# Kernel tuning notes

Measured on AMD Instinct MI355X. Metric: run time of the kernel, lower is better.

The kernel has to match this reference:

```python
import jax, jax.numpy as jnp
import numpy as np

D_MODEL = 1024
N_HEADS = 16
D_HEAD = D_MODEL // N_HEADS
SCALE = 1.0 / (D_HEAD ** 0.5)


def _rel_shift(t):
    # Transformer-XL relative shift: pad -> view -> slice -> view. t: [b,h,q,k]
    b, h, q, k = t.shape
    padded = jnp.pad(t, ((0, 0), (0, 0), (0, 0), (1, 0)))  # [b,h,q,k+1]
    shifted = padded.reshape(b, h, k + 1, q)[:, :, 1:, :].reshape(b, h, q, k)
    return shifted


def setup_inputs() -> dict:
    key = jax.random.key(0)
    ks = jax.random.split(key, 10)
    B, T, M = 2, 1024, 1024
    J = M + T
    inp = {
        "x": jax.random.normal(ks[0], (B, T, D_MODEL), dtype=jnp.float32),
        "memory": jax.random.normal(ks[1], (B, M, D_MODEL), dtype=jnp.float32),
        "pos_emb": jax.random.normal(ks[2], (J, D_MODEL), dtype=jnp.float32),
        # nn.Linear(d, d, bias=False) weights: y = x @ W.T, W: [out, in]
        "q_w": jax.random.normal(ks[3], (D_MODEL, D_MODEL), dtype=jnp.float32) * 0.02,
        "k_w": jax.random.normal(ks[4], (D_MODEL, D_MODEL), dtype=jnp.float32) * 0.02,
        "v_w": jax.random.normal(ks[5], (D_MODEL, D_MODEL), dtype=jnp.float32) * 0.02,
        "r_w": jax.random.normal(ks[6], (D_MODEL, D_MODEL), dtype=jnp.float32) * 0.02,
        "out_w": jax.random.normal(ks[7], (D_MODEL, D_MODEL), dtype=jnp.float32) * 0.02,
        "pos_bias_u": jax.random.normal(ks[8], (N_HEADS, D_HEAD), dtype=jnp.float32) * 0.02,
        "pos_bias_v": jax.random.normal(ks[9], (N_HEADS, D_HEAD), dtype=jnp.float32) * 0.02,
    }
    return inp


def reference(x, memory, pos_emb, q_w, k_w, v_w, r_w, out_w, pos_bias_u, pos_bias_v):
    B, T, _ = x.shape
    cat = jnp.concatenate([memory, x], axis=1)  # [B, M+T, d]
    L = cat.shape[1]

    def heads(t):  # [B, time, d] -> [B, h, time, dh]
        return t.reshape(t.shape[0], t.shape[1], N_HEADS, D_HEAD).transpose(0, 2, 1, 3)

    q = heads(x @ q_w.T)      # [B,h,T,dh]
    k = heads(cat @ k_w.T)    # [B,h,L,dh]
    v = heads(cat @ v_w.T)    # [B,h,L,dh]
    r = (pos_emb @ r_w.T).reshape(-1, N_HEADS, D_HEAD).transpose(1, 0, 2)  # [h,J,dh]

    q_u = q + pos_bias_u[None, :, None, :]
    q_v = q + pos_bias_v[None, :, None, :]

    content_score = jnp.einsum('bhqd,bhkd->bhqk', q_u, k)  # [B,h,T,L]
    rel_score = jnp.einsum('bhqd,hjd->bhqj', q_v, r)        # [B,h,T,J]
    rel_score = _rel_shift(rel_score)

    scores = (content_score + rel_score) * SCALE
    attn = jax.nn.softmax(scores, axis=-1)
    out = jnp.einsum('bhqk,bhkd->bhqd', attn, v)            # [B,h,T,dh]
    out = out.transpose(0, 2, 1, 3).reshape(B, T, N_HEADS * D_HEAD)
    return out @ out_w.T
```

## Files before the change

kernel.cpp:

```cpp
#include <hip/hip_runtime.h>


typedef unsigned short u16;
typedef unsigned int u32;
typedef short bf16x8 __attribute__((ext_vector_type(8)));
typedef float f32x4 __attribute__((ext_vector_type(4)));

#define MFMA16(a, b, c) __builtin_amdgcn_mfma_f32_16x16x32_bf16(a, b, c, 0, 0, 0)

__device__ __forceinline__ u16 f2bf(float f) {
  u32 u = __float_as_uint(f);
  u32 r = (u + 0x7fffu + ((u >> 16) & 1u)) >> 16;
  return (u16)r;
}

__device__ __forceinline__ void async16(void* lds, const void* g) {
  __builtin_amdgcn_global_load_lds(
      (const __attribute__((address_space(1))) u32*)g,
      (__attribute__((address_space(3))) u32*)lds, 16, 0, 0);
}

__global__ void prep_kernel(const float* __restrict__ x, const float* __restrict__ mem,
                            const float* __restrict__ pos,
                            const float* __restrict__ qw, const float* __restrict__ kw,
                            const float* __restrict__ vw, const float* __restrict__ rw,
                            const float* __restrict__ ow,
                            u16* __restrict__ catb, u16* __restrict__ posb,
                            u16* __restrict__ wqb, u16* __restrict__ wkb,
                            u16* __restrict__ wvb, u16* __restrict__ wrb,
                            u16* __restrict__ wob) {
  const int seg = blockIdx.y;
  const int vid = blockIdx.x * blockDim.x + threadIdx.x;
  const float* src = nullptr;
  u16* dst = nullptr;
  int count = 0;
  switch (seg) {
    case 0: count = (2 * 2048 * 1024) / 4; dst = catb; break;
    case 1: count = (2048 * 1024) / 4; src = pos; dst = posb; break;
    case 2: count = (1024 * 1024) / 4; src = qw; dst = wqb; break;
    case 3: count = (1024 * 1024) / 4; src = kw; dst = wkb; break;
    case 4: count = (1024 * 1024) / 4; src = vw; dst = wvb; break;
    case 5: count = (1024 * 1024) / 4; src = rw; dst = wrb; break;
    case 6: count = (1024 * 1024) / 4; src = ow; dst = wob; break;
  }
  if (vid >= count) return;
  float4 f;
  if (seg == 0) {
    int e = vid * 4;
    int col = e & 1023;
    int row = (e >> 10) & 2047;
    int b = e >> 21;
    const float* s2 = (row < 1024)
                          ? (mem + ((size_t)(b * 1024 + row) * 1024 + col))
                          : (x + ((size_t)(b * 1024 + (row - 1024)) * 1024 + col));
    f = *(const float4*)s2;
  } else {
    f = *(const float4*)(src + (size_t)vid * 4);
  }
  ushort4 o4;
  o4.x = f2bf(f.x); o4.y = f2bf(f.y); o4.z = f2bf(f.z); o4.w = f2bf(f.w);
  *(ushort4*)(dst + (size_t)vid * 4) = o4;
}

__device__ __forceinline__ void gemm_core(const u16* __restrict__ A, const u16* __restrict__ W,
                                          u16* As, u16* Bs, int m0, int n0, bool qmap,
                                          f32x4 acc[4][4]) {
  const int t = threadIdx.x;
  const int lane = t & 63, wid = t >> 6;
  const int colL = lane & 15, rg = lane >> 4;
  const int wm = (wid >> 1) * 64, wn = (wid & 1) * 64;
  for (int kt = 0; kt < 32; ++kt) {
    __syncthreads();
#pragma unroll
    for (int pass = 0; pass < 2; ++pass) {
      int slot = t + pass * 256;
      int row = slot >> 2, ch = slot & 3;
      int sch = ch ^ ((row >> 1) & 3);
      int ar = m0 + row;
      if (qmap) ar = ((ar >> 10) << 11) + 1024 + (ar & 1023);
      async16(As + slot * 8, A + (size_t)ar * 1024 + kt * 32 + sch * 8);
      async16(Bs + slot * 8, W + (size_t)(n0 + row) * 1024 + kt * 32 + sch * 8);
    }
    __syncthreads();
    bf16x8 af[4], bfr[4];
#pragma unroll
    for (int mi = 0; mi < 4; ++mi) {
      int r = wm + mi * 16 + colL;
      af[mi] = *(const bf16x8*)(As + r * 32 + (rg ^ ((r >> 1) & 3)) * 8);
    }
#pragma unroll
    for (int ni = 0; ni < 4; ++ni) {
      int r = wn + ni * 16 + colL;
      bfr[ni] = *(const bf16x8*)(Bs + r * 32 + (rg ^ ((r >> 1) & 3)) * 8);
    }
#pragma unroll
    for (int mi = 0; mi < 4; ++mi)
#pragma unroll
      for (int ni = 0; ni < 4; ++ni)
        acc[mi][ni] = MFMA16(af[mi], bfr[ni], acc[mi][ni]);
  }
}

__global__ __launch_bounds__(256, 2) void gemm_qkvr(
    const u16* __restrict__ catb, const u16* __restrict__ posb,
    const u16* __restrict__ wqb, const u16* __restrict__ wrb,
    const u16* __restrict__ wkb, const u16* __restrict__ wvb,
    const float* __restrict__ bu, const float* __restrict__ bv,
    u16* __restrict__ qub, u16* __restrict__ qvb, u16* __restrict__ rbuf,
    u16* __restrict__ kbuf, u16* __restrict__ vtbuf) {
  __shared__ u16 As[128 * 32], Bs[128 * 32];
  __shared__ u16 Ep[4][16 * 72];
  const int x = blockIdx.x;
  const int bid = (x & 7) * 96 + (x >> 3);
  const u16* A;
  const u16* W;
  int mode, r2;
  bool qmap = false;
  if (bid < 128)      { mode = 0; A = catb; W = wqb; qmap = true; r2 = bid; }
  else if (bid < 256) { mode = 1; A = posb; W = wrb; r2 = bid - 128; }
  else if (bid < 512) { mode = 2; A = catb; W = wkb; r2 = bid - 256; }
  else                { mode = 3; A = catb; W = wvb; r2 = bid - 512; }
  const int m0 = (r2 >> 3) * 128, n0 = (r2 & 7) * 128;
  f32x4 acc[4][4];
  f32x4 zz = {0.f, 0.f, 0.f, 0.f};
#pragma unroll
  for (int a1 = 0; a1 < 4; ++a1)
#pragma unroll
    for (int a2 = 0; a2 < 4; ++a2) acc[a1][a2] = zz;
  gemm_core(A, W, As, Bs, m0, n0, qmap, acc);
  const int t = threadIdx.x, lane = t & 63, wid = t >> 6;
  const int colL = lane & 15, rg = lane >> 4;
  const int wm = (wid >> 1) * 64, wn = (wid & 1) * 64;
  const float sc = 0.18033688f;
  if (mode == 3) {
    u16* Ew = &Ep[wid][0];
    const int bb = m0 >> 11;
    const int j0w = (m0 + wm) & 2047;
    const int hh = (n0 + wn) >> 6;
    const size_t vb0 =
        (((size_t)(bb * 16 + hh) * 32 + (j0w >> 6)) * 4) * 1024;
#pragma unroll
    for (int ni = 0; ni < 4; ++ni) {
#pragma unroll
      for (int mi = 0; mi < 4; ++mi) {
        u32 lo = (u32)f2bf(acc[mi][ni][0]) | ((u32)f2bf(acc[mi][ni][1]) << 16);
        u32 hi = (u32)f2bf(acc[mi][ni][2]) | ((u32)f2bf(acc[mi][ni][3]) << 16);
        uint2 pk; pk.x = lo; pk.y = hi;
        *(uint2*)(Ew + colL * 72 + mi * 16 + rg * 4) = pk;
      }
      asm volatile("s_waitcnt lgkmcnt(0)" ::: "memory");
      const size_t vb = vb0 + (size_t)ni * 1024;
#pragma unroll
      for (int rr = 0; rr < 2; ++rr) {
        int ch = rr * 4 + rg;
        int dr = colL;
        bf16x8 vv = *(const bf16x8*)(Ew + dr * 72 + ch * 8);
        *(bf16x8*)(vtbuf + vb + ch * 128 + dr * 8) = vv;
      }
      asm volatile("s_waitcnt lgkmcnt(0)" ::: "memory");
    }
    return;
  }
#pragma unroll
  for (int mi = 0; mi < 4; ++mi)
#pragma unroll
    for (int ni = 0; ni < 4; ++ni)
#pragma unroll
      for (int e = 0; e < 4; ++e) {
        int m = m0 + wm + mi * 16 + rg * 4 + e;
        int n = n0 + wn + ni * 16 + colL;
        float val = acc[mi][ni][e];
        int hh = n >> 6, dd = n & 63;
        if (mode == 0) {
          int bb = m >> 10, tq = m & 1023;
          size_t ad = (((size_t)(bb * 16 + hh)) * 1024 + tq) * 64 + dd;
          qub[ad] = f2bf((val + bu[n]) * sc);
          qvb[ad] = f2bf((val + bv[n]) * sc);
        } else if (mode == 1) {
          rbuf[((((size_t)hh * 128 + (m >> 4)) * 8 + (dd >> 3)) * 16 + (m & 15)) * 8 +
               (dd & 7)] = f2bf(val);
        } else {
          int bb = m >> 11, j = m & 2047;
          size_t bh2 = (size_t)(bb * 16 + hh);
          kbuf[(((bh2 * 128 + (j >> 4)) * 8 + (dd >> 3)) * 16 + (j & 15)) * 8 + (dd & 7)] =
              f2bf(val);
        }
      }
}

__global__ __launch_bounds__(256, 2) void attn_kernel(
    const u16* __restrict__ qu, const u16* __restrict__ qv, const u16* __restrict__ ktile,
    const u16* __restrict__ vtile, const u16* __restrict__ rtile,
    float* __restrict__ opart, float* __restrict__ mlpart) {
  __shared__ float Ulds[4][3200];
  const int t = threadIdx.x;
  const int wid = t >> 6, lane = t & 63;
  const int colL = lane & 15, rg = lane >> 4;
  const int bid = ((blockIdx.x & 7) << 6) | (blockIdx.x >> 3);
  const int bh = bid >> 4;
  const int rem = bid & 15;
  const int qc = rem >> 1, ks = rem & 1;
  const int h = bh & 15;
  const int i0 = qc * 128 + wid * 32;

  const u16* qub = qu + (size_t)bh * (1024 * 64);
  const u16* qvb = qv + (size_t)bh * (1024 * 64);
  const u16* kb = ktile + (size_t)bh * (128 * 1024);
  const u16* vb = vtile + (size_t)bh * (32 * 4096);
  const u16* rb = rtile + (size_t)h * (128 * 1024);
  const int lane8 = (rg * 16 + colL) * 8;

  bf16x8 aqu0[2], aqv0[2], aqu1[2], aqv1[2];
  {
    int r0 = i0 + colL;
    int r1 = i0 + 16 + colL;
#pragma unroll
    for (int kx = 0; kx < 2; ++kx) {
      aqu0[kx] = *(const bf16x8*)(qub + (size_t)r0 * 64 + kx * 32 + rg * 8);
      aqv0[kx] = *(const bf16x8*)(qvb + (size_t)r0 * 64 + kx * 32 + rg * 8);
      aqu1[kx] = *(const bf16x8*)(qub + (size_t)r1 * 64 + kx * 32 + rg * 8);
      aqv1[kx] = *(const bf16x8*)(qvb + (size_t)r1 * 64 + kx * 32 + rg * 8);
    }
  }
  bf16x8 ones;
#pragma unroll
  for (int i = 0; i < 8; ++i) ones[i] = (short)0x3F80;

  const f32x4 zz = {0.f, 0.f, 0.f, 0.f};
  f32x4 o0[4], o1[4];
  f32x4 lacc0 = zz, lacc1 = zz;
#pragma unroll
  for (int e = 0; e < 4; ++e) { o0[e] = zz; o1[e] = zz; }
  int lb0[4], lb1[4];
#pragma unroll
  for (int e = 0; e < 4; ++e) {
    lb0[e] = (rg * 4 + e) * 99 + colL + 31;
    lb1[e] = (rg * 4 + e) * 99 + colL + 1615;
  }

  float* Uw = &Ulds[wid][0];
  u16* Pw = (u16*)Uw;

#pragma unroll 1
  for (int jt = ks * 16; jt < ks * 16 + 16; ++jt) {
    const int j0 = jt * 64;
    f32x4 s0[4], s1[4];
    __builtin_amdgcn_s_setprio(1);
#pragma unroll
    for (int ni = 0; ni < 4; ++ni) {
      const u16* kp = kb + (size_t)((j0 >> 4) + ni) * 1024 + lane8;
      bf16x8 b0 = *(const bf16x8*)kp;
      bf16x8 b1 = *(const bf16x8*)(kp + 512);
      s0[ni] = zz;
      s0[ni] = MFMA16(aqu0[0], b0, s0[ni]);
      s0[ni] = MFMA16(aqu0[1], b1, s0[ni]);
      s1[ni] = zz;
      s1[ni] = MFMA16(aqu1[0], b0, s1[ni]);
      s1[ni] = MFMA16(aqu1[1], b1, s1[ni]);
    }
    __builtin_amdgcn_s_setprio(0);
    const int pbase2 = j0 + 992 - i0;
    const bool mainv = (pbase2 <= 2047);
    const bool leak = (pbase2 + 94 >= 2049);
    if (mainv) {
      const int tb = pbase2 >> 4;
      bf16x8 rc[12];
#pragma unroll
      for (int uc = 0; uc < 6; ++uc) {
        int tt = tb + uc;
        tt = tt < 127 ? tt : 127;
        const u16* rp = rb + (size_t)tt * 1024 + lane8;
        rc[2 * uc] = *(const bf16x8*)rp;
        rc[2 * uc + 1] = *(const bf16x8*)(rp + 512);
      }
      __builtin_amdgcn_s_setprio(1);
#pragma unroll
      for (int uc = 1; uc < 6; ++uc) {
        f32x4 ua = zz;
        ua = MFMA16(aqv0[0], rc[2 * uc], ua);
        ua = MFMA16(aqv0[1], rc[2 * uc + 1], ua);
#pragma unroll
        for (int e = 0; e < 4; ++e) Uw[(rg * 4 + e) * 100 + uc * 16 + colL] = ua[e];
      }
#pragma unroll
      for (int uc = 0; uc < 5; ++uc) {
        f32x4 ub = zz;
        ub = MFMA16(aqv1[0], rc[2 * uc], ub);
        ub = MFMA16(aqv1[1], rc[2 * uc + 1], ub);
#pragma unroll
        for (int e = 0; e < 4; ++e) Uw[(16 + rg * 4 + e) * 100 + uc * 16 + colL] = ub[e];
      }
      __builtin_amdgcn_s_setprio(0);
      asm volatile("s_waitcnt lgkmcnt(0)" ::: "memory");
      const int pl0 = pbase2 + colL + 31;
      const int pl1 = pbase2 + colL + 15;
#pragma unroll
      for (int c = 0; c < 4; ++c)
#pragma unroll
        for (int e = 0; e < 4; ++e) {
          int w0e = rg * 4 + e;
          float u0 = Uw[lb0[e] + c * 16];
          float u1 = Uw[lb1[e] + c * 16];
          int p0 = pl0 + c * 16 - w0e;
          int p1 = pl1 + c * 16 - w0e;
          s0[c][e] += (p0 <= 2047) ? u0 : 0.f;
          s1[c][e] += (p1 <= 2047) ? u1 : 0.f;
        }
    }
    if (leak) {
      asm volatile("s_waitcnt lgkmcnt(0)" ::: "memory");
      bf16x8 aqs0[2], aqs1[2];
      {
        int rs0 = i0 + colL + 1;
        int rs1 = i0 + 16 + colL + 1;
        rs1 = rs1 < 1024 ? rs1 : 1023;
#pragma unroll
        for (int kx = 0; kx < 2; ++kx) {
          aqs0[kx] = *(const bf16x8*)(qvb + (size_t)rs0 * 64 + kx * 32 + rg * 8);
          aqs1[kx] = *(const bf16x8*)(qvb + (size_t)rs1 * 64 + kx * 32 + rg * 8);
        }
      }
      const int mB1 = (pbase2 - 2048) >> 4;
      const int rowL = (colL + 15) & 15;
      const int tadj = (colL > 0) ? 0 : -1;
      bf16x8 r2[12];
#pragma unroll
      for (int uc = 0; uc < 6; ++uc) {
        int tL = mB1 + uc + tadj;
        tL = tL < 0 ? 0 : (tL > 127 ? 127 : tL);
        const u16* rp = rb + (size_t)tL * 1024 + rg * 128 + rowL * 8;
        r2[2 * uc] = *(const bf16x8*)rp;
        r2[2 * uc + 1] = *(const bf16x8*)(rp + 512);
      }
      __builtin_amdgcn_s_setprio(1);
#pragma unroll
      for (int uc = 1; uc < 6; ++uc) {
        f32x4 ua = zz;
        ua = MFMA16(aqs0[0], r2[2 * uc], ua);
        ua = MFMA16(aqs0[1], r2[2 * uc + 1], ua);
#pragma unroll
        for (int e = 0; e < 4; ++e) Uw[(rg * 4 + e) * 100 + uc * 16 + colL] = ua[e];
      }
#pragma unroll
      for (int uc = 0; uc < 5; ++uc) {
        f32x4 ub = zz;
        ub = MFMA16(aqs1[0], r2[2 * uc], ub);
        ub = MFMA16(aqs1[1], r2[2 * uc + 1], ub);
#pragma unroll
        for (int e = 0; e < 4; ++e) Uw[(16 + rg * 4 + e) * 100 + uc * 16 + colL] = ub[e];
      }
      __builtin_amdgcn_s_setprio(0);
      asm volatile("s_waitcnt lgkmcnt(0)" ::: "memory");
      const int pl0 = pbase2 + colL + 31;
      const int pl1 = pbase2 + colL + 15;
#pragma unroll
      for (int c = 0; c < 4; ++c)
#pragma unroll
        for (int e = 0; e < 4; ++e) {
          int w0e = rg * 4 + e;
          int p0 = pl0 + c * 16 - w0e;
          int p1 = pl1 + c * 16 - w0e;
          if (p0 >= 2049) s0[c][e] += Uw[lb0[e] + c * 16];
          if (p1 >= 2049) s1[c][e] += Uw[lb1[e] + c * 16];
        }
    }
    bf16x8 vf[8];
    {
      const u16* vp0 = vb + (size_t)jt * 4096 + lane8;
#pragma unroll
      for (int ni = 0; ni < 4; ++ni) {
        vf[2 * ni] = *(const bf16x8*)(vp0 + ni * 1024);
        vf[2 * ni + 1] = *(const bf16x8*)(vp0 + ni * 1024 + 512);
      }
    }
#pragma unroll
    for (int c = 0; c < 4; ++c)
#pragma unroll
      for (int e = 0; e < 4; ++e) {
        int row = rg * 4 + e;
        int col = c * 16 + colL;
        int sw = (col >> 3) ^ (row & 7);
        float p0 = __builtin_amdgcn_exp2f(s0[c][e] - 16.0f);
        float p1 = __builtin_amdgcn_exp2f(s1[c][e] - 16.0f);
        Pw[row * 64 + sw * 8 + (colL & 7)] = f2bf(p0);
        Pw[(16 + row) * 64 + sw * 8 + (colL & 7)] = f2bf(p1);
      }
    asm volatile("s_waitcnt lgkmcnt(0)" ::: "memory");
    bf16x8 pa0[2], pa1[2];
#pragma unroll
    for (int kx = 0; kx < 2; ++kx) {
      int chunk = kx * 4 + rg;
      int sw = chunk ^ (colL & 7);
      pa0[kx] = *(const bf16x8*)(Pw + colL * 64 + sw * 8);
      pa1[kx] = *(const bf16x8*)(Pw + (16 + colL) * 64 + sw * 8);
    }
    __builtin_amdgcn_s_setprio(1);
    lacc0 = MFMA16(pa0[0], ones, lacc0);
    lacc0 = MFMA16(pa0[1], ones, lacc0);
    lacc1 = MFMA16(pa1[0], ones, lacc1);
    lacc1 = MFMA16(pa1[1], ones, lacc1);
#pragma unroll
    for (int ni = 0; ni < 4; ++ni) {
      o0[ni] = MFMA16(pa0[0], vf[2 * ni], o0[ni]);
      o0[ni] = MFMA16(pa0[1], vf[2 * ni + 1], o0[ni]);
      o1[ni] = MFMA16(pa1[0], vf[2 * ni], o1[ni]);
      o1[ni] = MFMA16(pa1[1], vf[2 * ni + 1], o1[ni]);
    }
    __builtin_amdgcn_s_setprio(0);
    asm volatile("" ::: "memory");
  }
  const size_t rowbase = (size_t)ks * 32768 + (size_t)bh * 1024 + i0;
#pragma unroll
  for (int c = 0; c < 4; ++c)
#pragma unroll
    for (int e = 0; e < 4; ++e) {
      int row = rg * 4 + e;
      opart[(rowbase + row) * 64 + c * 16 + colL] = o0[c][e];
      opart[(rowbase + 16 + row) * 64 + c * 16 + colL] = o1[c][e];
    }
  if (colL == 0) {
#pragma unroll
    for (int e = 0; e < 4; ++e) {
      size_t r = rowbase + rg * 4 + e;
      mlpart[r * 2 + 0] = 16.0f;
      mlpart[r * 2 + 1] = lacc0[e];
      mlpart[(r + 16) * 2 + 0] = 16.0f;
      mlpart[(r + 16) * 2 + 1] = lacc1[e];
    }
  }
}

__global__ void combine_kernel(const float* __restrict__ opart,
                               const float* __restrict__ mlpart,
                               u16* __restrict__ aout) {
  const int gid = blockIdx.x * 256 + threadIdx.x;
  const int r = gid >> 4;
  const int cg = gid & 15;
  float2 ml0 = *(const float2*)(mlpart + (size_t)r * 2);
  float2 ml1 = *(const float2*)(mlpart + ((size_t)32768 + r) * 2);
  float m = fmaxf(ml0.x, ml1.x);
  float f0 = __builtin_amdgcn_exp2f(ml0.x - m);
  float f1 = __builtin_amdgcn_exp2f(ml1.x - m);
  float inv = 1.0f / (ml0.y * f0 + ml1.y * f1);
  f0 *= inv; f1 *= inv;
  float4 a = *(const float4*)(opart + (size_t)r * 64 + cg * 4);
  float4 b4 = *(const float4*)(opart + ((size_t)32768 + r) * 64 + cg * 4);
  ushort4 o4;
  o4.x = f2bf(a.x * f0 + b4.x * f1);
  o4.y = f2bf(a.y * f0 + b4.y * f1);
  o4.z = f2bf(a.z * f0 + b4.z * f1);
  o4.w = f2bf(a.w * f0 + b4.w * f1);
  const int bh = r >> 10, i = r & 1023;
  const int b = bh >> 4, h = bh & 15;
  *(ushort4*)(aout + ((size_t)(b * 1024 + i) * 1024 + h * 64 + cg * 4)) = o4;
}

__global__ __launch_bounds__(256, 2) void gemm_out(
    const u16* __restrict__ aob, const u16* __restrict__ wob, float* __restrict__ out) {
  __shared__ u16 As[128 * 32], Bs[128 * 32];
  const int bid = ((blockIdx.x & 7) << 4) | (blockIdx.x >> 3);
  const int mt = bid >> 3, nt = bid & 7;
  const int m0 = mt * 128, n0 = nt * 128;
  f32x4 acc[4][4];
  f32x4 zz = {0.f, 0.f, 0.f, 0.f};
#pragma unroll
  for (int a1 = 0; a1 < 4; ++a1)
#pragma unroll
    for (int a2 = 0; a2 < 4; ++a2) acc[a1][a2] = zz;
  gemm_core(aob, wob, As, Bs, m0, n0, false, acc);
  const int t = threadIdx.x, lane = t & 63, wid = t >> 6;
  const int colL = lane & 15, rg = lane >> 4;
  const int wm = (wid >> 1) * 64, wn = (wid & 1) * 64;
#pragma unroll
  for (int mi = 0; mi < 4; ++mi)
#pragma unroll
    for (int ni = 0; ni < 4; ++ni)
#pragma unroll
      for (int e = 0; e < 4; ++e) {
        int m = m0 + wm + mi * 16 + rg * 4 + e;
        int n = n0 + wn + ni * 16 + colL;
        out[(size_t)m * 1024 + n] = acc[mi][ni][e];
      }
}

extern "C" void kernel_launch(void* const* d_in, const int* in_sizes, int n_in,
                              void* d_out, int out_size, void* d_ws, size_t ws_size,
                              hipStream_t stream) {
  (void)in_sizes; (void)n_in; (void)out_size; (void)ws_size;
  const float* x = (const float*)d_in[0];
  const float* mem = (const float*)d_in[1];
  const float* pos = (const float*)d_in[2];
  const float* qw = (const float*)d_in[3];
  const float* kw = (const float*)d_in[4];
  const float* vw = (const float*)d_in[5];
  const float* rw = (const float*)d_in[6];
  const float* ow = (const float*)d_in[7];
  const float* bu = (const float*)d_in[8];
  const float* bv = (const float*)d_in[9];
  float* out = (float*)d_out;

  char* w = (char*)d_ws;
  u16* catb = (u16*)(w + 0);
  u16* posb = (u16*)(w + 8388608);
  u16* wqb  = (u16*)(w + 12582912);
  u16* wkb  = (u16*)(w + 14680064);
  u16* wvb  = (u16*)(w + 16777216);
  u16* wrb  = (u16*)(w + 18874368);
  u16* wob  = (u16*)(w + 20971520);
  u16* qub  = (u16*)(w + 23068672);
  u16* qvb  = (u16*)(w + 27262976);
  u16* kbuf = (u16*)(w + 31457280);
  u16* vtb  = (u16*)(w + 39845888);
  u16* rbuf = (u16*)(w + 48234496);
  u16* aob  = (u16*)(w + 52428800);
  float* opart  = (float*)(w + 0);
  float* mlpart = (float*)(w + 16777216);

  prep_kernel<<<dim3(4096, 7), 256, 0, stream>>>(x, mem, pos, qw, kw, vw, rw, ow,
                                                 catb, posb, wqb, wkb, wvb, wrb, wob);
  gemm_qkvr<<<768, 256, 0, stream>>>(catb, posb, wqb, wrb, wkb, wvb, bu, bv,
                                     qub, qvb, rbuf, kbuf, vtb);
  attn_kernel<<<512, 256, 0, stream>>>(qub, qvb, kbuf, vtb, rbuf, opart, mlpart);
  combine_kernel<<<2048, 256, 0, stream>>>(opart, mlpart, aob);
  gemm_out<<<128, 256, 0, stream>>>(aob, wob, out);
}
```

Baseline: 227.5 us.

## Fuse fp32-to-bf16 conversion into GEMMs and merge split-K combine into output GEMM

Removes the separate prep kernel by having the QKVR and output GEMMs load fp32 inputs and weights directly, convert them to bf16 in registers, and stage them into LDS with register prefetch of the next K tile. This replaces the async global-to-LDS loads. The combine kernel is folded into the output GEMM's A-tile load, which sums the two split-K partials and divides by the summed row normaliser. It also drops the constant max from the partial output, keeping only the row sums, and removes the s_setprio hints in the attention kernel. This saves two launches and the bf16 intermediate round-trips, at the cost of reading fp32 data (double the bytes) repeatedly across tiles and more VALU conversion work inside the GEMM main loops.

```diff
diff --git a/kernel.cpp b/kernel.cpp
--- a/kernel.cpp
+++ b/kernel.cpp
@@ -14,131 +14,121 @@
   return (u16)r;
 }
 
-__device__ __forceinline__ void async16(void* lds, const void* g) {
-  __builtin_amdgcn_global_load_lds(
-      (const __attribute__((address_space(1))) u32*)g,
-      (__attribute__((address_space(3))) u32*)lds, 16, 0, 0);
+__device__ __forceinline__ bf16x8 cvt8(float4 a, float4 b) {
+  bf16x8 r;
+  r[0] = (short)f2bf(a.x); r[1] = (short)f2bf(a.y);
+  r[2] = (short)f2bf(a.z); r[3] = (short)f2bf(a.w);
+  r[4] = (short)f2bf(b.x); r[5] = (short)f2bf(b.y);
+  r[6] = (short)f2bf(b.z); r[7] = (short)f2bf(b.w);
+  return r;
 }
 
-__global__ void prep_kernel(const float* __restrict__ x, const float* __restrict__ mem,
-                            const float* __restrict__ pos,
-                            const float* __restrict__ qw, const float* __restrict__ kw,
-                            const float* __restrict__ vw, const float* __restrict__ rw,
-                            const float* __restrict__ ow,
-                            u16* __restrict__ catb, u16* __restrict__ posb,
-                            u16* __restrict__ wqb, u16* __restrict__ wkb,
-                            u16* __restrict__ wvb, u16* __restrict__ wrb,
-                            u16* __restrict__ wob) {
-  const int seg = blockIdx.y;
-  const int vid = blockIdx.x * blockDim.x + threadIdx.x;
-  const float* src = nullptr;
-  u16* dst = nullptr;
-  int count = 0;
-  switch (seg) {
-    case 0: count = (2 * 2048 * 1024) / 4; dst = catb; break;
-    case 1: count = (2048 * 1024) / 4; src = pos; dst = posb; break;
-    case 2: count = (1024 * 1024) / 4; src = qw; dst = wqb; break;
-    case 3: count = (1024 * 1024) / 4; src = kw; dst = wkb; break;
-    case 4: count = (1024 * 1024) / 4; src = vw; dst = wvb; break;
-    case 5: count = (1024 * 1024) / 4; src = rw; dst = wrb; break;
-    case 6: count = (1024 * 1024) / 4; src = ow; dst = wob; break;
-  }
-  if (vid >= count) return;
-  float4 f;
-  if (seg == 0) {
-    int e = vid * 4;
-    int col = e & 1023;
-    int row = (e >> 10) & 2047;
-    int b = e >> 21;
-    const float* s2 = (row < 1024)
-                          ? (mem + ((size_t)(b * 1024 + row) * 1024 + col))
-                          : (x + ((size_t)(b * 1024 + (row - 1024)) * 1024 + col));
-    f = *(const float4*)s2;
-  } else {
-    f = *(const float4*)(src + (size_t)vid * 4);
-  }
-  ushort4 o4;
-  o4.x = f2bf(f.x); o4.y = f2bf(f.y); o4.z = f2bf(f.z); o4.w = f2bf(f.w);
-  *(ushort4*)(dst + (size_t)vid * 4) = o4;
-}
-
-__device__ __forceinline__ void gemm_core(const u16* __restrict__ A, const u16* __restrict__ W,
-                                          u16* As, u16* Bs, int m0, int n0, bool qmap,
-                                          f32x4 acc[4][4]) {
-  const int t = threadIdx.x;
-  const int lane = t & 63, wid = t >> 6;
-  const int colL = lane & 15, rg = lane >> 4;
-  const int wm = (wid >> 1) * 64, wn = (wid & 1) * 64;
-  for (int kt = 0; kt < 32; ++kt) {
-    __syncthreads();
-#pragma unroll
-    for (int pass = 0; pass < 2; ++pass) {
-      int slot = t + pass * 256;
-      int row = slot >> 2, ch = slot & 3;
-      int sch = ch ^ ((row >> 1) & 3);
-      int ar = m0 + row;
-      if (qmap) ar = ((ar >> 10) << 11) + 1024 + (ar & 1023);
-      async16(As + slot * 8, A + (size_t)ar * 1024 + kt * 32 + sch * 8);
-      async16(Bs + slot * 8, W + (size_t)(n0 + row) * 1024 + kt * 32 + sch * 8);
-    }
-    __syncthreads();
-    bf16x8 af[4], bfr[4];
-#pragma unroll
-    for (int mi = 0; mi < 4; ++mi) {
-      int r = wm + mi * 16 + colL;
-      af[mi] = *(const bf16x8*)(As + r * 32 + (rg ^ ((r >> 1) & 3)) * 8);
-    }
-#pragma unroll
-    for (int ni = 0; ni < 4; ++ni) {
-      int r = wn + ni * 16 + colL;
-      bfr[ni] = *(const bf16x8*)(Bs + r * 32 + (rg ^ ((r >> 1) & 3)) * 8);
-    }
-#pragma unroll
-    for (int mi = 0; mi < 4; ++mi)
-#pragma unroll
-      for (int ni = 0; ni < 4; ++ni)
-        acc[mi][ni] = MFMA16(af[mi], bfr[ni], acc[mi][ni]);
-  }
-}
-
 __global__ __launch_bounds__(256, 2) void gemm_qkvr(
-    const u16* __restrict__ catb, const u16* __restrict__ posb,
-    const u16* __restrict__ wqb, const u16* __restrict__ wrb,
-    const u16* __restrict__ wkb, const u16* __restrict__ wvb,
+    const float* __restrict__ x, const float* __restrict__ mem,
+    const float* __restrict__ pos,
+    const float* __restrict__ qw, const float* __restrict__ kw,
+    const float* __restrict__ vw, const float* __restrict__ rw,
     const float* __restrict__ bu, const float* __restrict__ bv,
     u16* __restrict__ qub, u16* __restrict__ qvb, u16* __restrict__ rbuf,
     u16* __restrict__ kbuf, u16* __restrict__ vtbuf) {
   __shared__ u16 As[128 * 32], Bs[128 * 32];
   __shared__ u16 Ep[4][16 * 72];
-  const int x = blockIdx.x;
-  const int bid = (x & 7) * 96 + (x >> 3);
-  const u16* A;
-  const u16* W;
+  const int xb = blockIdx.x;
+  const int bid = (xb & 7) * 96 + (xb >> 3);
   int mode, r2;
-  bool qmap = false;
-  if (bid < 128)      { mode = 0; A = catb; W = wqb; qmap = true; r2 = bid; }
-  else if (bid < 256) { mode = 1; A = posb; W = wrb; r2 = bid - 128; }
-  else if (bid < 512) { mode = 2; A = catb; W = wkb; r2 = bid - 256; }
-  else                { mode = 3; A = catb; W = wvb; r2 = bid - 512; }
+  const float* Wsrc;
+  if (bid < 128)      { mode = 0; Wsrc = qw; r2 = bid; }
+  else if (bid < 256) { mode = 1; Wsrc = rw; r2 = bid - 128; }
+  else if (bid < 512) { mode = 2; Wsrc = kw; r2 = bid - 256; }
+  else                { mode = 3; Wsrc = vw; r2 = bid - 512; }
   const int m0 = (r2 >> 3) * 128, n0 = (r2 & 7) * 128;
-  f32x4 acc[4][4];
-  f32x4 zz = {0.f, 0.f, 0.f, 0.f};
-#pragma unroll
-  for (int a1 = 0; a1 < 4; ++a1)
-#pragma unroll
-    for (int a2 = 0; a2 < 4; ++a2) acc[a1][a2] = zz;
-  gemm_core(A, W, As, Bs, m0, n0, qmap, acc);
   const int t = threadIdx.x, lane = t & 63, wid = t >> 6;
   const int colL = lane & 15, rg = lane >> 4;
   const int wm = (wid >> 1) * 64, wn = (wid & 1) * 64;
+
+  const float* arow[2];
+  const float* wrow[2];
+  int schs[2];
+#pragma unroll
+  for (int pass = 0; pass < 2; ++pass) {
+    int slot = t + pass * 256;
+    int row = slot >> 2, ch = slot & 3;
+    schs[pass] = ch ^ ((row >> 1) & 3);
+    int ar = m0 + row;
+    if (mode == 0) {
+      int b = ar >> 10;
+      arow[pass] = x + ((size_t)(b * 1024 + (ar & 1023))) * 1024;
+    } else if (mode == 1) {
+      arow[pass] = pos + (size_t)ar * 1024;
+    } else {
+      int b = ar >> 11, j = ar & 2047;
+      arow[pass] = (j < 1024) ? mem + ((size_t)(b * 1024 + j)) * 1024
+                              : x + ((size_t)(b * 1024 + j - 1024)) * 1024;
+    }
+    wrow[pass] = Wsrc + (size_t)(n0 + row) * 1024;
+  }
+
+  f32x4 acc[4][4];
+  f32x4 zz = {0.f, 0.f, 0.f, 0.f};
+#pragma unroll
+  for (int a1 = 0; a1 < 4; ++a1)
+#pragma unroll
+    for (int a2 = 0; a2 < 4; ++a2) acc[a1][a2] = zz;
+
+  float4 ra[2][2], rb[2][2];
+#pragma unroll
+  for (int pass = 0; pass < 2; ++pass) {
+    int col = schs[pass] * 8;
+    ra[pass][0] = *(const float4*)(arow[pass] + col);
+    ra[pass][1] = *(const float4*)(arow[pass] + col + 4);
+    rb[pass][0] = *(const float4*)(wrow[pass] + col);
+    rb[pass][1] = *(const float4*)(wrow[pass] + col + 4);
+  }
+#pragma unroll 1
+  for (int kt = 0; kt < 32; ++kt) {
+    __syncthreads();
+#pragma unroll
+    for (int pass = 0; pass < 2; ++pass) {
+      int slot = t + pass * 256;
+      *(bf16x8*)(As + slot * 8) = cvt8(ra[pass][0], ra[pass][1]);
+      *(bf16x8*)(Bs + slot * 8) = cvt8(rb[pass][0], rb[pass][1]);
+    }
+    __syncthreads();
+    if (kt < 31) {
+#pragma unroll
+      for (int pass = 0; pass < 2; ++pass) {
+        int col = (kt + 1) * 32 + schs[pass] * 8;
+        ra[pass][0] = *(const float4*)(arow[pass] + col);
+        ra[pass][1] = *(const float4*)(arow[pass] + col + 4);
+        rb[pass][0] = *(const float4*)(wrow[pass] + col);
+        rb[pass][1] = *(const float4*)(wrow[pass] + col + 4);
+      }
+    }
+    bf16x8 af[4], bfr[4];
+#pragma unroll
+    for (int mi = 0; mi < 4; ++mi) {
+      int r = wm + mi * 16 + colL;
+      af[mi] = *(const bf16x8*)(As + r * 32 + (rg ^ ((r >> 1) & 3)) * 8);
+    }
+#pragma unroll
+    for (int ni = 0; ni < 4; ++ni) {
+      int r = wn + ni * 16 + colL;
+      bfr[ni] = *(const bf16x8*)(Bs + r * 32 + (rg ^ ((r >> 1) & 3)) * 8);
+    }
+#pragma unroll
+    for (int mi = 0; mi < 4; ++mi)
+#pragma unroll
+      for (int ni = 0; ni < 4; ++ni)
+        acc[mi][ni] = MFMA16(af[mi], bfr[ni], acc[mi][ni]);
+  }
+
   const float sc = 0.18033688f;
   if (mode == 3) {
     u16* Ew = &Ep[wid][0];
     const int bb = m0 >> 11;
     const int j0w = (m0 + wm) & 2047;
     const int hh = (n0 + wn) >> 6;
-    const size_t vb0 =
-        (((size_t)(bb * 16 + hh) * 32 + (j0w >> 6)) * 4) * 1024;
+    const size_t vb0 = (((size_t)(bb * 16 + hh) * 32 + (j0w >> 6)) * 4) * 1024;
 #pragma unroll
     for (int ni = 0; ni < 4; ++ni) {
 #pragma unroll
@@ -153,9 +143,8 @@
 #pragma unroll
       for (int rr = 0; rr < 2; ++rr) {
         int ch = rr * 4 + rg;
-        int dr = colL;
-        bf16x8 vv = *(const bf16x8*)(Ew + dr * 72 + ch * 8);
-        *(bf16x8*)(vtbuf + vb + ch * 128 + dr * 8) = vv;
+        bf16x8 vv = *(const bf16x8*)(Ew + colL * 72 + ch * 8);
+        *(bf16x8*)(vtbuf + vb + ch * 128 + colL * 8) = vv;
       }
       asm volatile("s_waitcnt lgkmcnt(0)" ::: "memory");
     }
@@ -191,7 +180,7 @@
 __global__ __launch_bounds__(256, 2) void attn_kernel(
     const u16* __restrict__ qu, const u16* __restrict__ qv, const u16* __restrict__ ktile,
     const u16* __restrict__ vtile, const u16* __restrict__ rtile,
-    float* __restrict__ opart, float* __restrict__ mlpart) {
+    float* __restrict__ opart, float* __restrict__ lpart) {
   __shared__ float Ulds[4][3200];
   const int t = threadIdx.x;
   const int wid = t >> 6, lane = t & 63;
@@ -245,7 +234,6 @@
   for (int jt = ks * 16; jt < ks * 16 + 16; ++jt) {
     const int j0 = jt * 64;
     f32x4 s0[4], s1[4];
-    __builtin_amdgcn_s_setprio(1);
 #pragma unroll
     for (int ni = 0; ni < 4; ++ni) {
       const u16* kp = kb + (size_t)((j0 >> 4) + ni) * 1024 + lane8;
@@ -258,7 +246,6 @@
       s1[ni] = MFMA16(aqu1[0], b0, s1[ni]);
       s1[ni] = MFMA16(aqu1[1], b1, s1[ni]);
     }
-    __builtin_amdgcn_s_setprio(0);
     const int pbase2 = j0 + 992 - i0;
     const bool mainv = (pbase2 <= 2047);
     const bool leak = (pbase2 + 94 >= 2049);
@@ -273,7 +260,6 @@
         rc[2 * uc] = *(const bf16x8*)rp;
         rc[2 * uc + 1] = *(const bf16x8*)(rp + 512);
       }
-      __builtin_amdgcn_s_setprio(1);
 #pragma unroll
       for (int uc = 1; uc < 6; ++uc) {
         f32x4 ua = zz;
@@ -290,7 +276,6 @@
 #pragma unroll
         for (int e = 0; e < 4; ++e) Uw[(16 + rg * 4 + e) * 100 + uc * 16 + colL] = ub[e];
       }
-      __builtin_amdgcn_s_setprio(0);
       asm volatile("s_waitcnt lgkmcnt(0)" ::: "memory");
       const int pl0 = pbase2 + colL + 31;
       const int pl1 = pbase2 + colL + 15;
@@ -332,7 +317,6 @@
         r2[2 * uc] = *(const bf16x8*)rp;
         r2[2 * uc + 1] = *(const bf16x8*)(rp + 512);
       }
-      __builtin_amdgcn_s_setprio(1);
 #pragma unroll
       for (int uc = 1; uc < 6; ++uc) {
         f32x4 ua = zz;
@@ -349,7 +333,6 @@
 #pragma unroll
         for (int e = 0; e < 4; ++e) Uw[(16 + rg * 4 + e) * 100 + uc * 16 + colL] = ub[e];
       }
-      __builtin_amdgcn_s_setprio(0);
       asm volatile("s_waitcnt lgkmcnt(0)" ::: "memory");
       const int pl0 = pbase2 + colL + 31;
       const int pl1 = pbase2 + colL + 15;
@@ -394,7 +377,6 @@
       pa0[kx] = *(const bf16x8*)(Pw + colL * 64 + sw * 8);
       pa1[kx] = *(const bf16x8*)(Pw + (16 + colL) * 64 + sw * 8);
     }
-    __builtin_amdgcn_s_setprio(1);
     lacc0 = MFMA16(pa0[0], ones, lacc0);
     lacc0 = MFMA16(pa0[1], ones, lacc0);
     lacc1 = MFMA16(pa1[0], ones, lacc1);
@@ -406,7 +388,6 @@
       o1[ni] = MFMA16(pa1[0], vf[2 * ni], o1[ni]);
       o1[ni] = MFMA16(pa1[1], vf[2 * ni + 1], o1[ni]);
     }
-    __builtin_amdgcn_s_setprio(0);
     asm volatile("" ::: "memory");
   }
   const size_t rowbase = (size_t)ks * 32768 + (size_t)bh * 1024 + i0;
@@ -422,55 +403,121 @@
 #pragma unroll
     for (int e = 0; e < 4; ++e) {
       size_t r = rowbase + rg * 4 + e;
-      mlpart[r * 2 + 0] = 16.0f;
-      mlpart[r * 2 + 1] = lacc0[e];
-      mlpart[(r + 16) * 2 + 0] = 16.0f;
-      mlpart[(r + 16) * 2 + 1] = lacc1[e];
+      lpart[r] = lacc0[e];
+      lpart[r + 16] = lacc1[e];
     }
   }
 }
 
-__global__ void combine_kernel(const float* __restrict__ opart,
-                               const float* __restrict__ mlpart,
-                               u16* __restrict__ aout) {
-  const int gid = blockIdx.x * 256 + threadIdx.x;
-  const int r = gid >> 4;
-  const int cg = gid & 15;
-  float2 ml0 = *(const float2*)(mlpart + (size_t)r * 2);
-  float2 ml1 = *(const float2*)(mlpart + ((size_t)32768 + r) * 2);
-  float m = fmaxf(ml0.x, ml1.x);
-  float f0 = __builtin_amdgcn_exp2f(ml0.x - m);
-  float f1 = __builtin_amdgcn_exp2f(ml1.x - m);
-  float inv = 1.0f / (ml0.y * f0 + ml1.y * f1);
-  f0 *= inv; f1 *= inv;
-  float4 a = *(const float4*)(opart + (size_t)r * 64 + cg * 4);
-  float4 b4 = *(const float4*)(opart + ((size_t)32768 + r) * 64 + cg * 4);
-  ushort4 o4;
-  o4.x = f2bf(a.x * f0 + b4.x * f1);
-  o4.y = f2bf(a.y * f0 + b4.y * f1);
-  o4.z = f2bf(a.z * f0 + b4.z * f1);
-  o4.w = f2bf(a.w * f0 + b4.w * f1);
-  const int bh = r >> 10, i = r & 1023;
-  const int b = bh >> 4, h = bh & 15;
-  *(ushort4*)(aout + ((size_t)(b * 1024 + i) * 1024 + h * 64 + cg * 4)) = o4;
-}
-
 __global__ __launch_bounds__(256, 2) void gemm_out(
-    const u16* __restrict__ aob, const u16* __restrict__ wob, float* __restrict__ out) {
+    const float* __restrict__ opart, const float* __restrict__ lpart,
+    const float* __restrict__ ow, float* __restrict__ out) {
   __shared__ u16 As[128 * 32], Bs[128 * 32];
   const int bid = ((blockIdx.x & 7) << 4) | (blockIdx.x >> 3);
   const int mt = bid >> 3, nt = bid & 7;
   const int m0 = mt * 128, n0 = nt * 128;
-  f32x4 acc[4][4];
-  f32x4 zz = {0.f, 0.f, 0.f, 0.f};
-#pragma unroll
-  for (int a1 = 0; a1 < 4; ++a1)
-#pragma unroll
-    for (int a2 = 0; a2 < 4; ++a2) acc[a1][a2] = zz;
-  gemm_core(aob, wob, As, Bs, m0, n0, false, acc);
   const int t = threadIdx.x, lane = t & 63, wid = t >> 6;
   const int colL = lane & 15, rg = lane >> 4;
   const int wm = (wid >> 1) * 64, wn = (wid & 1) * 64;
+
+  int rowm[2], schs[2];
+  const float* wrow[2];
+#pragma unroll
+  for (int pass = 0; pass < 2; ++pass) {
+    int slot = t + pass * 256;
+    int row = slot >> 2, ch = slot & 3;
+    schs[pass] = ch ^ ((row >> 1) & 3);
+    rowm[pass] = m0 + row;
+    wrow[pass] = ow + (size_t)(n0 + row) * 1024;
+  }
+
+  f32x4 acc[4][4];
+  f32x4 zz = {0.f, 0.f, 0.f, 0.f};
+#pragma unroll
+  for (int a1 = 0; a1 < 4; ++a1)
+#pragma unroll
+    for (int a2 = 0; a2 < 4; ++a2) acc[a1][a2] = zz;
+
+  float4 ra[2][2], rb[2][2];
+  float rl[2];
+#pragma unroll
+  for (int pass = 0; pass < 2; ++pass) {
+    int c = schs[pass] * 8;
+    int m = rowm[pass];
+    int b = m >> 10, i = m & 1023;
+    size_t r = ((size_t)(b * 16 + (c >> 6))) * 1024 + i;
+    int dd = c & 63;
+    ra[pass][0] = *(const float4*)(opart + r * 64 + dd);
+    ra[pass][1] = *(const float4*)(opart + (32768 + r) * 64 + dd);
+    rl[pass] = lpart[r] + lpart[32768 + r];
+    rb[pass][0] = *(const float4*)(wrow[pass] + c);
+    rb[pass][1] = *(const float4*)(wrow[pass] + c + 4);
+  }
+  float4 ra2[2][2];
+#pragma unroll
+  for (int pass = 0; pass < 2; ++pass) {
+    int c = schs[pass] * 8;
+    int m = rowm[pass];
+    int b = m >> 10, i = m & 1023;
+    size_t r = ((size_t)(b * 16 + (c >> 6))) * 1024 + i;
+    int dd = c & 63;
+    ra2[pass][0] = *(const float4*)(opart + r * 64 + dd + 4);
+    ra2[pass][1] = *(const float4*)(opart + (32768 + r) * 64 + dd + 4);
+  }
+#pragma unroll 1
+  for (int kt = 0; kt < 32; ++kt) {
+    __syncthreads();
+#pragma unroll
+    for (int pass = 0; pass < 2; ++pass) {
+      int slot = t + pass * 256;
+      float inv = 1.0f / rl[pass];
+      float4 lo, hi;
+      lo.x = (ra[pass][0].x + ra[pass][1].x) * inv;
+      lo.y = (ra[pass][0].y + ra[pass][1].y) * inv;
+      lo.z = (ra[pass][0].z + ra[pass][1].z) * inv;
+      lo.w = (ra[pass][0].w + ra[pass][1].w) * inv;
+      hi.x = (ra2[pass][0].x + ra2[pass][1].x) * inv;
+      hi.y = (ra2[pass][0].y + ra2[pass][1].y) * inv;
+      hi.z = (ra2[pass][0].z + ra2[pass][1].z) * inv;
+      hi.w = (ra2[pass][0].w + ra2[pass][1].w) * inv;
+      *(bf16x8*)(As + slot * 8) = cvt8(lo, hi);
+      *(bf16x8*)(Bs + slot * 8) = cvt8(rb[pass][0], rb[pass][1]);
+    }
+    __syncthreads();
+    if (kt < 31) {
+#pragma unroll
+      for (int pass = 0; pass < 2; ++pass) {
+        int c = (kt + 1) * 32 + schs[pass] * 8;
+        int m = rowm[pass];
+        int b = m >> 10, i = m & 1023;
+        size_t r = ((size_t)(b * 16 + (c >> 6))) * 1024 + i;
+        int dd = c & 63;
+        ra[pass][0] = *(const float4*)(opart + r * 64 + dd);
+        ra[pass][1] = *(const float4*)(opart + (32768 + r) * 64 + dd);
+        ra2[pass][0] = *(const float4*)(opart + r * 64 + dd + 4);
+        ra2[pass][1] = *(const float4*)(opart + (32768 + r) * 64 + dd + 4);
+        rl[pass] = lpart[r] + lpart[32768 + r];
+        rb[pass][0] = *(const float4*)(wrow[pass] + c);
+        rb[pass][1] = *(const float4*)(wrow[pass] + c + 4);
+      }
+    }
+    bf16x8 af[4], bfr[4];
+#pragma unroll
+    for (int mi = 0; mi < 4; ++mi) {
+      int r = wm + mi * 16 + colL;
+      af[mi] = *(const bf16x8*)(As + r * 32 + (rg ^ ((r >> 1) & 3)) * 8);
+    }
+#pragma unroll
+    for (int ni = 0; ni < 4; ++ni) {
+      int r = wn + ni * 16 + colL;
+      bfr[ni] = *(const bf16x8*)(Bs + r * 32 + (rg ^ ((r >> 1) & 3)) * 8);
+    }
+#pragma unroll
+    for (int mi = 0; mi < 4; ++mi)
+#pragma unroll
+      for (int ni = 0; ni < 4; ++ni)
+        acc[mi][ni] = MFMA16(af[mi], bfr[ni], acc[mi][ni]);
+  }
 #pragma unroll
   for (int mi = 0; mi < 4; ++mi)
 #pragma unroll
@@ -500,27 +547,16 @@
   float* out = (float*)d_out;
 
   char* w = (char*)d_ws;
-  u16* catb = (u16*)(w + 0);
-  u16* posb = (u16*)(w + 8388608);
-  u16* wqb  = (u16*)(w + 12582912);
-  u16* wkb  = (u16*)(w + 14680064);
-  u16* wvb  = (u16*)(w + 16777216);
-  u16* wrb  = (u16*)(w + 18874368);
-  u16* wob  = (u16*)(w + 20971520);
+  float* opart = (float*)(w + 0);
+  float* lpart = (float*)(w + 16777216);
   u16* qub  = (u16*)(w + 23068672);
   u16* qvb  = (u16*)(w + 27262976);
   u16* kbuf = (u16*)(w + 31457280);
   u16* vtb  = (u16*)(w + 39845888);
   u16* rbuf = (u16*)(w + 48234496);
-  u16* aob  = (u16*)(w + 52428800);
-  float* opart  = (float*)(w + 0);
-  float* mlpart = (float*)(w + 16777216);
-
-  prep_kernel<<<dim3(4096, 7), 256, 0, stream>>>(x, mem, pos, qw, kw, vw, rw, ow,
-                                                 catb, posb, wqb, wkb, wvb, wrb, wob);
-  gemm_qkvr<<<768, 256, 0, stream>>>(catb, posb, wqb, wrb, wkb, wvb, bu, bv,
+
+  gemm_qkvr<<<768, 256, 0, stream>>>(x, mem, pos, qw, kw, vw, rw, bu, bv,
                                      qub, qvb, rbuf, kbuf, vtb);
-  attn_kernel<<<512, 256, 0, stream>>>(qub, qvb, kbuf, vtb, rbuf, opart, mlpart);
-  combine_kernel<<<2048, 256, 0, stream>>>(opart, mlpart, aob);
-  gemm_out<<<128, 256, 0, stream>>>(aob, wob, out);
+  attn_kernel<<<512, 256, 0, stream>>>(qub, qvb, kbuf, vtb, rbuf, opart, lpart);
+  gemm_out<<<128, 256, 0, stream>>>(opart, lpart, ow, out);
 }
```

New measurement: 251.3 us. +10.5%, slower.
